# Performance work log

Measured on AMD Instinct MI355X. Metric: run time of the kernel, lower is better.

The kernel has to match this reference:

```python
import jax, jax.numpy as jnp
import numpy as np


def setup_inputs() -> dict:
    key = jax.random.key(0)
    kP, kd, ke, kp, kw = jax.random.split(key, 5)
    B, L, Q, E = 64, 128, 128, 16384  # batch, logical qubits, physical qubits, circuit edges
    P = jax.random.uniform(kP, (B, L, Q), dtype=jnp.float32)
    d_hw = jax.random.randint(kd, (Q, Q), 0, 4).astype(jnp.float32)  # hardware distances; ==1 means adjacent
    d_error = jax.random.uniform(ke, (Q, Q), dtype=jnp.float32)      # 2Q gate error in [0,1)
    circuit_edge_pairs = jax.random.randint(kp, (E, 2), 0, L, dtype=jnp.int32)
    circuit_edge_weights = jax.random.uniform(kw, (E,), dtype=jnp.float32)
    return {
        "P": P,
        "d_hw": d_hw,
        "d_error": d_error,
        "circuit_edge_pairs": circuit_edge_pairs,
        "circuit_edge_weights": circuit_edge_weights,
    }


def reference(P, d_hw, d_error, circuit_edge_pairs, circuit_edge_weights):
    # A_fidelity[p,q] = 1{d_hw==1} * max(1 - d_error, 0)
    A_fid = (d_hw == 1.0).astype(P.dtype) * jnp.maximum(1.0 - d_error, 0.0)  # [Q,Q]
    # Gather endpoints for every circuit edge: [B,E,Q]
    Pi = P[:, circuit_edge_pairs[:, 0], :]
    Pj = P[:, circuit_edge_pairs[:, 1], :]
    # adj_score[b,e] = sum_{p,q} Pi[b,e,p] * A_fid[p,q] * Pj[b,e,q]
    scores = jnp.einsum("bep,pq,beq->be", Pi, A_fid, Pj)  # [B,E]
    mean_scores = scores.mean(axis=0)                      # [E] (mean over batch, as in .mean())
    w = circuit_edge_weights
    total_weight = jnp.maximum(w.sum(), 1e-8)
    loss = -(w * mean_scores).sum() / total_weight
    return loss
```

## Files before the change

### kernel.cpp

```cpp
#include <hip/hip_runtime.h>

#define NB 64
#define NL 128
#define NQ 128
#define NE 16384

#define WS_TW    0
#define WS_PART  8
#define WS_W     272
#define US_ATB   33312

using short8 = __attribute__((ext_vector_type(8))) short;
using f32x4  = __attribute__((ext_vector_type(4))) float;

__device__ inline unsigned short f2bf(float f) {
    const unsigned u = __float_as_uint(f);
    return (unsigned short)((u + 0x7fffu + ((u >> 16) & 1u)) >> 16);
}

__device__ inline short8 pack8(float4 a, float4 b) {
    short8 r;
    r[0] = f2bf(a.x); r[1] = f2bf(a.y); r[2] = f2bf(a.z); r[3] = f2bf(a.w);
    r[4] = f2bf(b.x); r[5] = f2bf(b.y); r[6] = f2bf(b.z); r[7] = f2bf(b.w);
    return r;
}

__global__ __launch_bounds__(512) void prep_kernel(const float* __restrict__ dhw,
                                                   const float* __restrict__ derr,
                                                   const int*  __restrict__ pairs,
                                                   const float* __restrict__ wts,
                                                   float* __restrict__ ws) {
    const int t = threadIdx.x, blk = blockIdx.x;

    if (blk < 8) {
        __shared__ float Wl[16 * 132];
        __shared__ float red[8];
        const int oct = blk;
        for (int idx = t; idx < 16 * 132; idx += 512) Wl[idx] = 0.f;
        __syncthreads();

        float tw = 0.f;
        #pragma unroll 4
        for (int r = 0; r < 32; ++r) {
            const int e = t + 512 * r;
            const int2  pr = ((const int2*)pairs)[e];
            const float w  = wts[e];
            tw += w;
            if ((pr.x >> 4) == oct)
                atomicAdd(&Wl[(pr.x & 15) * 132 + pr.y], w);
        }
        __syncthreads();

        #pragma unroll
        for (int r = 0; r < 4; ++r) {
            const int idx = t + 512 * r;
            const int row = idx >> 7, col = idx & 127;
            ws[WS_W + oct * 2048 + idx] = Wl[row * 132 + col];
        }

        if (oct == 0) {
            #pragma unroll
            for (int off = 32; off; off >>= 1) tw += __shfl_down(tw, off, 64);
            if ((t & 63) == 0) red[t >> 6] = tw;
            __syncthreads();
            if (t == 0) {
                float s = 0.f;
                #pragma unroll
                for (int k = 0; k < 8; ++k) s += red[k];
                ws[WS_TW] = s;
            }
        }
    } else {
        unsigned short* us = (unsigned short*)ws;
        #pragma unroll
        for (int r = 0; r < 4; ++r) {
            const int idx = (blk - 8) * 2048 + t + 512 * r;
            const float hw = dhw[idx], er = derr[idx];
            const float a  = (hw == 1.0f) ? fmaxf(1.0f - er, 0.f) : 0.f;
            const int p = idx >> 7, q = idx & 127;
            us[US_ATB + q * 128 + p] = f2bf(a);
        }
    }
}

__global__ __launch_bounds__(512) void main_kernel(const float* __restrict__ P,
                                                   float* __restrict__ ws) {
    __shared__ unsigned short Pbl[128 * 136];
    __shared__ float redS[8];

    const int t   = threadIdx.x;
    const int blk = blockIdx.x;
    const int b   = blk >> 2;
    const int qtr = blk & 3;
    const float* __restrict__ Pb = P + b * 16384;
    const unsigned short* us = (const unsigned short*)ws;

    float4 pv[8];
    #pragma unroll
    for (int r = 0; r < 8; ++r) pv[r] = ((const float4*)Pb)[t + 512 * r];
    #pragma unroll
    for (int r = 0; r < 8; ++r) {
        const int f   = t + 512 * r;
        const int row = f >> 5, c4 = (f & 31) * 4;
        ushort4 u;
        u.x = f2bf(pv[r].x); u.y = f2bf(pv[r].y);
        u.z = f2bf(pv[r].z); u.w = f2bf(pv[r].w);
        *(ushort4*)&Pbl[row * 136 + c4] = u;
    }
    __syncthreads();

    const int wv   = t >> 6;
    const int lane = t & 63;
    const int l15  = lane & 15;
    const int kb   = (lane >> 4) * 8;
    const int ncol = wv * 16 + l15;

    short8 gb8[4], yb8[4];
    #pragma unroll
    for (int kk = 0; kk < 4; ++kk) {
        const int k0 = kk * 32 + kb;
        short8 g;
        #pragma unroll
        for (int d = 0; d < 8; ++d)
            g[d] = (short)Pbl[(k0 + d) * 136 + ncol];
        gb8[kk] = g;
        yb8[kk] = *(const short8*)&us[US_ATB + ncol * 128 + k0];
    }

    float s = 0.f;
    #pragma unroll
    for (int uu = 0; uu < 2; ++uu) {
        const int mrow = qtr * 32 + uu * 16 + l15;
        const float* __restrict__ Wrow = ws + WS_W + mrow * 128;
        f32x4 accG = {0.f, 0.f, 0.f, 0.f};
        f32x4 accY = {0.f, 0.f, 0.f, 0.f};
        #pragma unroll
        for (int kk = 0; kk < 4; ++kk) {
            const int k0 = kk * 32 + kb;
            const short8 wa = pack8(*(const float4*)&Wrow[k0],
                                    *(const float4*)&Wrow[k0 + 4]);
            const short8 pa = *(const short8*)&Pbl[mrow * 136 + k0];
            accG = __builtin_amdgcn_mfma_f32_16x16x32_bf16(wa, gb8[kk], accG, 0, 0, 0);
            accY = __builtin_amdgcn_mfma_f32_16x16x32_bf16(pa, yb8[kk], accY, 0, 0, 0);
        }
        s += accG[0] * accY[0] + accG[1] * accY[1]
           + accG[2] * accY[2] + accG[3] * accY[3];
    }

    #pragma unroll
    for (int off = 32; off; off >>= 1) s += __shfl_down(s, off, 64);
    if (lane == 0) redS[wv] = s;
    __syncthreads();
    if (t == 0) {
        float ss = 0.f;
        #pragma unroll
        for (int k = 0; k < 8; ++k) ss += redS[k];
        ws[WS_PART + blk] = ss;
    }
}

__global__ __launch_bounds__(256) void finalize_kernel(const float* __restrict__ ws,
                                                       float* __restrict__ out) {
    const int t = threadIdx.x, lane = t & 63, wv = t >> 6;
    float n = ws[WS_PART + t];
    #pragma unroll
    for (int off = 32; off; off >>= 1) n += __shfl_down(n, off, 64);
    __shared__ float red[4];
    if (lane == 0) red[wv] = n;
    __syncthreads();
    if (t == 0) {
        const float num = red[0] + red[1] + red[2] + red[3];
        out[0] = -num / ((float)NB * fmaxf(ws[WS_TW], 1e-8f));
    }
}

extern "C" void kernel_launch(void* const* d_in, const int* in_sizes, int n_in,
                              void* d_out, int out_size, void* d_ws, size_t ws_size,
                              hipStream_t stream) {
    const float* P    = (const float*)d_in[0];
    const float* dhw  = (const float*)d_in[1];
    const float* derr = (const float*)d_in[2];
    const int*   prs  = (const int*)d_in[3];
    const float* wts  = (const float*)d_in[4];
    float* ws  = (float*)d_ws;
    float* out = (float*)d_out;

    prep_kernel<<<16, 512, 0, stream>>>(dhw, derr, prs, wts, ws);
    main_kernel<<<256, 512, 0, stream>>>(P, ws);
    finalize_kernel<<<1, 256, 0, stream>>>(ws, out);
}
```

Before: 22.66 us.

## Precompute bf16 P and its transpose in prep kernel, main reads from workspace

Moves the fp32-to-bf16 conversion of P into the prep kernel, which writes both a row-major and a transposed bf16 copy to the workspace. The edge-weight matrix W is also stored as bf16. The main kernel then loads MFMA operands directly from global memory and no longer stages through LDS or needs a barrier. The aim is to stop the four blocks per batch from each reconverting and staging all of P. In exchange it adds about 4 MB of extra global writes and reads, and prep grows from 16 to 80 blocks, which likely lengthens the serial prep stage.

```diff
diff --git a/kernel.cpp b/kernel.cpp
--- a/kernel.cpp
+++ b/kernel.cpp
@@ -7,8 +7,10 @@
 
 #define WS_TW    0
 #define WS_PART  8
-#define WS_W     272
-#define US_ATB   33312
+#define US_WB    544
+#define US_ATB   (US_WB + 16384)
+#define US_PB    (US_ATB + 16384)
+#define US_PTB   (US_PB + NB * 16384)
 
 using short8 = __attribute__((ext_vector_type(8))) short;
 using f32x4  = __attribute__((ext_vector_type(4))) float;
@@ -18,24 +20,47 @@
     return (unsigned short)((u + 0x7fffu + ((u >> 16) & 1u)) >> 16);
 }
 
-__device__ inline short8 pack8(float4 a, float4 b) {
-    short8 r;
-    r[0] = f2bf(a.x); r[1] = f2bf(a.y); r[2] = f2bf(a.z); r[3] = f2bf(a.w);
-    r[4] = f2bf(b.x); r[5] = f2bf(b.y); r[6] = f2bf(b.z); r[7] = f2bf(b.w);
-    return r;
-}
-
-__global__ __launch_bounds__(512) void prep_kernel(const float* __restrict__ dhw,
+__global__ __launch_bounds__(512) void prep_kernel(const float* __restrict__ P,
+                                                   const float* __restrict__ dhw,
                                                    const float* __restrict__ derr,
                                                    const int*  __restrict__ pairs,
                                                    const float* __restrict__ wts,
                                                    float* __restrict__ ws) {
     const int t = threadIdx.x, blk = blockIdx.x;
+    unsigned short* us = (unsigned short*)ws;
 
-    if (blk < 8) {
+    if (blk < 64) {
+        const float* __restrict__ Pb = P + blk * 16384;
+        unsigned short* __restrict__ PBb  = us + US_PB  + blk * 16384;
+        unsigned short* __restrict__ PTBb = us + US_PTB + blk * 16384;
+        __shared__ unsigned short T[128 * 132];
+
+        #pragma unroll
+        for (int r = 0; r < 8; ++r) {
+            const int f = t + 512 * r;
+            const float4 v = ((const float4*)Pb)[f];
+            ushort4 u;
+            u.x = f2bf(v.x); u.y = f2bf(v.y); u.z = f2bf(v.z); u.w = f2bf(v.w);
+            ((ushort4*)PBb)[f] = u;
+            const int i = f >> 5, c = (f & 31) * 4;
+            *(ushort4*)&T[i * 132 + c] = u;
+        }
+        __syncthreads();
+        #pragma unroll
+        for (int r = 0; r < 4; ++r) {
+            const int o  = t + 512 * r;
+            const int q  = o & 127;
+            const int j0 = (o >> 7) * 8;
+            short8 rd;
+            #pragma unroll
+            for (int d = 0; d < 8; ++d)
+                rd[d] = (short)T[(j0 + d) * 132 + q];
+            *(short8*)&PTBb[q * 128 + j0] = rd;
+        }
+    } else if (blk < 72) {
         __shared__ float Wl[16 * 132];
         __shared__ float red[8];
-        const int oct = blk;
+        const int oct = blk - 64;
         for (int idx = t; idx < 16 * 132; idx += 512) Wl[idx] = 0.f;
         __syncthreads();
 
@@ -55,7 +80,7 @@
         for (int r = 0; r < 4; ++r) {
             const int idx = t + 512 * r;
             const int row = idx >> 7, col = idx & 127;
-            ws[WS_W + oct * 2048 + idx] = Wl[row * 132 + col];
+            us[US_WB + oct * 2048 + idx] = f2bf(Wl[row * 132 + col]);
         }
 
         if (oct == 0) {
@@ -71,10 +96,9 @@
             }
         }
     } else {
-        unsigned short* us = (unsigned short*)ws;
         #pragma unroll
         for (int r = 0; r < 4; ++r) {
-            const int idx = (blk - 8) * 2048 + t + 512 * r;
+            const int idx = (blk - 72) * 2048 + t + 512 * r;
             const float hw = dhw[idx], er = derr[idx];
             const float a  = (hw == 1.0f) ? fmaxf(1.0f - er, 0.f) : 0.f;
             const int p = idx >> 7, q = idx & 127;
@@ -83,31 +107,18 @@
     }
 }
 
-__global__ __launch_bounds__(512) void main_kernel(const float* __restrict__ P,
+__global__ __launch_bounds__(512) void main_kernel(const float* __restrict__ ws_c,
                                                    float* __restrict__ ws) {
-    __shared__ unsigned short Pbl[128 * 136];
     __shared__ float redS[8];
-
     const int t   = threadIdx.x;
     const int blk = blockIdx.x;
     const int b   = blk >> 2;
     const int qtr = blk & 3;
-    const float* __restrict__ Pb = P + b * 16384;
-    const unsigned short* us = (const unsigned short*)ws;
-
-    float4 pv[8];
-    #pragma unroll
-    for (int r = 0; r < 8; ++r) pv[r] = ((const float4*)Pb)[t + 512 * r];
-    #pragma unroll
-    for (int r = 0; r < 8; ++r) {
-        const int f   = t + 512 * r;
-        const int row = f >> 5, c4 = (f & 31) * 4;
-        ushort4 u;
-        u.x = f2bf(pv[r].x); u.y = f2bf(pv[r].y);
-        u.z = f2bf(pv[r].z); u.w = f2bf(pv[r].w);
-        *(ushort4*)&Pbl[row * 136 + c4] = u;
-    }
-    __syncthreads();
+    const unsigned short* us = (const unsigned short*)ws_c;
+    const unsigned short* __restrict__ PBb  = us + US_PB  + b * 16384;
+    const unsigned short* __restrict__ PTBb = us + US_PTB + b * 16384;
+    const unsigned short* __restrict__ ATB  = us + US_ATB;
+    const unsigned short* __restrict__ WB   = us + US_WB;
 
     const int wv   = t >> 6;
     const int lane = t & 63;
@@ -119,27 +130,21 @@
     #pragma unroll
     for (int kk = 0; kk < 4; ++kk) {
         const int k0 = kk * 32 + kb;
-        short8 g;
-        #pragma unroll
-        for (int d = 0; d < 8; ++d)
-            g[d] = (short)Pbl[(k0 + d) * 136 + ncol];
-        gb8[kk] = g;
-        yb8[kk] = *(const short8*)&us[US_ATB + ncol * 128 + k0];
+        gb8[kk] = *(const short8*)&PTBb[ncol * 128 + k0];
+        yb8[kk] = *(const short8*)&ATB[ncol * 128 + k0];
     }
 
     float s = 0.f;
     #pragma unroll
     for (int uu = 0; uu < 2; ++uu) {
-        const int mrow = qtr * 32 + uu * 16 + l15;
-        const float* __restrict__ Wrow = ws + WS_W + mrow * 128;
+        const int mrow = (qtr * 2 + uu) * 16 + l15;
         f32x4 accG = {0.f, 0.f, 0.f, 0.f};
         f32x4 accY = {0.f, 0.f, 0.f, 0.f};
         #pragma unroll
         for (int kk = 0; kk < 4; ++kk) {
             const int k0 = kk * 32 + kb;
-            const short8 wa = pack8(*(const float4*)&Wrow[k0],
-                                    *(const float4*)&Wrow[k0 + 4]);
-            const short8 pa = *(const short8*)&Pbl[mrow * 136 + k0];
+            const short8 wa = *(const short8*)&WB[mrow * 128 + k0];
+            const short8 pa = *(const short8*)&PBb[mrow * 128 + k0];
             accG = __builtin_amdgcn_mfma_f32_16x16x32_bf16(wa, gb8[kk], accG, 0, 0, 0);
             accY = __builtin_amdgcn_mfma_f32_16x16x32_bf16(pa, yb8[kk], accY, 0, 0, 0);
         }
@@ -185,7 +190,7 @@
     float* ws  = (float*)d_ws;
     float* out = (float*)d_out;
 
-    prep_kernel<<<16, 512, 0, stream>>>(dhw, derr, prs, wts, ws);
-    main_kernel<<<256, 512, 0, stream>>>(P, ws);
+    prep_kernel<<<80, 512, 0, stream>>>(P, dhw, derr, prs, wts, ws);
+    main_kernel<<<256, 512, 0, stream>>>(ws, ws);
     finalize_kernel<<<1, 256, 0, stream>>>(ws, out);
 }
```

Result: slower. 24.44 us (+7.9%).

## Fuse finalize into main kernel via atomic counter; store edge-weight matrix as bf16

Applied to the files above, without the earlier changes.

Drops the separate finalize kernel. Each main-kernel block now atomically adds its partial sum, and the last block to arrive (found with an atomic counter) writes the loss. The prep kernel stores the weight matrix in bf16, so the main kernel loads half the bytes and skips the per-element conversion, and it reads pairs and weights with wider vector loads. This saves one kernel launch at the cost of float atomics, which make the summation order nondeterministic.

```diff
diff --git a/kernel.cpp b/kernel.cpp
--- a/kernel.cpp
+++ b/kernel.cpp
@@ -6,9 +6,10 @@
 #define NE 16384
 
 #define WS_TW    0
-#define WS_PART  8
-#define WS_W     272
-#define US_ATB   33312
+#define WS_NUM   1
+#define WS_CNT   2
+#define US_WB    544
+#define US_ATB   (US_WB + 16384)
 
 using short8 = __attribute__((ext_vector_type(8))) short;
 using f32x4  = __attribute__((ext_vector_type(4))) float;
@@ -18,19 +19,13 @@
     return (unsigned short)((u + 0x7fffu + ((u >> 16) & 1u)) >> 16);
 }
 
-__device__ inline short8 pack8(float4 a, float4 b) {
-    short8 r;
-    r[0] = f2bf(a.x); r[1] = f2bf(a.y); r[2] = f2bf(a.z); r[3] = f2bf(a.w);
-    r[4] = f2bf(b.x); r[5] = f2bf(b.y); r[6] = f2bf(b.z); r[7] = f2bf(b.w);
-    return r;
-}
-
 __global__ __launch_bounds__(512) void prep_kernel(const float* __restrict__ dhw,
                                                    const float* __restrict__ derr,
                                                    const int*  __restrict__ pairs,
                                                    const float* __restrict__ wts,
                                                    float* __restrict__ ws) {
     const int t = threadIdx.x, blk = blockIdx.x;
+    unsigned short* us = (unsigned short*)ws;
 
     if (blk < 8) {
         __shared__ float Wl[16 * 132];
@@ -41,13 +36,15 @@
 
         float tw = 0.f;
         #pragma unroll 4
-        for (int r = 0; r < 32; ++r) {
-            const int e = t + 512 * r;
-            const int2  pr = ((const int2*)pairs)[e];
-            const float w  = wts[e];
-            tw += w;
+        for (int r = 0; r < 16; ++r) {
+            const int e2 = t + 512 * r;
+            const int4   pr = ((const int4*)pairs)[e2];
+            const float2 w2 = ((const float2*)wts)[e2];
+            tw += w2.x + w2.y;
             if ((pr.x >> 4) == oct)
-                atomicAdd(&Wl[(pr.x & 15) * 132 + pr.y], w);
+                atomicAdd(&Wl[(pr.x & 15) * 132 + pr.y], w2.x);
+            if ((pr.z >> 4) == oct)
+                atomicAdd(&Wl[(pr.z & 15) * 132 + pr.w], w2.y);
         }
         __syncthreads();
 
@@ -55,7 +52,7 @@
         for (int r = 0; r < 4; ++r) {
             const int idx = t + 512 * r;
             const int row = idx >> 7, col = idx & 127;
-            ws[WS_W + oct * 2048 + idx] = Wl[row * 132 + col];
+            us[US_WB + oct * 2048 + idx] = f2bf(Wl[row * 132 + col]);
         }
 
         if (oct == 0) {
@@ -67,11 +64,12 @@
                 float s = 0.f;
                 #pragma unroll
                 for (int k = 0; k < 8; ++k) s += red[k];
-                ws[WS_TW] = s;
+                ws[WS_TW]  = s;
+                ws[WS_NUM] = 0.f;
+                ((int*)ws)[WS_CNT] = 0;
             }
         }
     } else {
-        unsigned short* us = (unsigned short*)ws;
         #pragma unroll
         for (int r = 0; r < 4; ++r) {
             const int idx = (blk - 8) * 2048 + t + 512 * r;
@@ -84,7 +82,8 @@
 }
 
 __global__ __launch_bounds__(512) void main_kernel(const float* __restrict__ P,
-                                                   float* __restrict__ ws) {
+                                                   float* __restrict__ ws,
+                                                   float* __restrict__ out) {
     __shared__ unsigned short Pbl[128 * 136];
     __shared__ float redS[8];
 
@@ -94,6 +93,8 @@
     const int qtr = blk & 3;
     const float* __restrict__ Pb = P + b * 16384;
     const unsigned short* us = (const unsigned short*)ws;
+    const unsigned short* __restrict__ ATB = us + US_ATB;
+    const unsigned short* __restrict__ WB  = us + US_WB;
 
     float4 pv[8];
     #pragma unroll
@@ -124,21 +125,19 @@
         for (int d = 0; d < 8; ++d)
             g[d] = (short)Pbl[(k0 + d) * 136 + ncol];
         gb8[kk] = g;
-        yb8[kk] = *(const short8*)&us[US_ATB + ncol * 128 + k0];
+        yb8[kk] = *(const short8*)&ATB[ncol * 128 + k0];
     }
 
     float s = 0.f;
     #pragma unroll
     for (int uu = 0; uu < 2; ++uu) {
         const int mrow = qtr * 32 + uu * 16 + l15;
-        const float* __restrict__ Wrow = ws + WS_W + mrow * 128;
         f32x4 accG = {0.f, 0.f, 0.f, 0.f};
         f32x4 accY = {0.f, 0.f, 0.f, 0.f};
         #pragma unroll
         for (int kk = 0; kk < 4; ++kk) {
             const int k0 = kk * 32 + kb;
-            const short8 wa = pack8(*(const float4*)&Wrow[k0],
-                                    *(const float4*)&Wrow[k0 + 4]);
+            const short8 wa = *(const short8*)&WB[mrow * 128 + k0];
             const short8 pa = *(const short8*)&Pbl[mrow * 136 + k0];
             accG = __builtin_amdgcn_mfma_f32_16x16x32_bf16(wa, gb8[kk], accG, 0, 0, 0);
             accY = __builtin_amdgcn_mfma_f32_16x16x32_bf16(pa, yb8[kk], accY, 0, 0, 0);
@@ -155,22 +154,14 @@
         float ss = 0.f;
         #pragma unroll
         for (int k = 0; k < 8; ++k) ss += redS[k];
-        ws[WS_PART + blk] = ss;
-    }
-}
-
-__global__ __launch_bounds__(256) void finalize_kernel(const float* __restrict__ ws,
-                                                       float* __restrict__ out) {
-    const int t = threadIdx.x, lane = t & 63, wv = t >> 6;
-    float n = ws[WS_PART + t];
-    #pragma unroll
-    for (int off = 32; off; off >>= 1) n += __shfl_down(n, off, 64);
-    __shared__ float red[4];
-    if (lane == 0) red[wv] = n;
-    __syncthreads();
-    if (t == 0) {
-        const float num = red[0] + red[1] + red[2] + red[3];
-        out[0] = -num / ((float)NB * fmaxf(ws[WS_TW], 1e-8f));
+        atomicAdd(&ws[WS_NUM], ss);
+        __threadfence();
+        const int old = atomicAdd((int*)ws + WS_CNT, 1);
+        if (old == 255) {
+            const float num = atomicAdd(&ws[WS_NUM], 0.0f);
+            const float tw  = fmaxf(ws[WS_TW], 1e-8f);
+            out[0] = -num / ((float)NB * tw);
+        }
     }
 }
 
@@ -186,6 +177,5 @@
     float* out = (float*)d_out;
 
     prep_kernel<<<16, 512, 0, stream>>>(dhw, derr, prs, wts, ws);
-    main_kernel<<<256, 512, 0, stream>>>(P, ws);
-    finalize_kernel<<<1, 256, 0, stream>>>(ws, out);
+    main_kernel<<<256, 512, 0, stream>>>(P, ws, out);
 }
```

Result: slower. 24.50 us (+8.1%).
